# Optimization experiments

Measured on AMD Instinct MI355X. Metric: run time of the kernel, lower is better.

The kernel has to match this reference:

```python
import jax, jax.numpy as jnp
import numpy as np

B, C_IN, N = 8, 3, 4096
H = [64, 128, 256]      # local conv widths
G = [128, 64]           # global MLP widths
K = 16                  # kNN neighbors for edge_conv
EPS = 1e-5


def _ln(x, g, b):
    # LayerNorm(num_point): normalize over the last (point) axis per channel
    mu = jnp.mean(x, axis=-1, keepdims=True)
    var = jnp.mean((x - mu) ** 2, axis=-1, keepdims=True)
    return (x - mu) / jnp.sqrt(var + EPS) * g + b


def _conv_ln_relu(x, w, b, g, be):
    # 1x1 Conv1d == per-point matmul: [B,Cin,N] -> [B,Cout,N]
    x = jnp.einsum('oi,bin->bon', w, x) + b[None, :, None]
    return jax.nn.relu(_ln(x, g, be))


def _edge_conv(x):
    # DGCNN-style edge conv: kNN in feature space, max-aggregate neighbor feats
    f = jnp.swapaxes(x, 1, 2)                                  # [B,N,C]
    sq = jnp.sum(f * f, axis=-1)                               # [B,N]
    d = sq[:, :, None] + sq[:, None, :] - 2.0 * jnp.einsum('bnc,bmc->bnm', f, f)
    _, idx = jax.lax.top_k(-jax.lax.stop_gradient(d), K)       # [B,N,K]
    nbr = jax.vmap(lambda fb, ib: fb[ib])(f, idx)              # [B,N,K,C] gather
    return jnp.swapaxes(jnp.max(nbr, axis=2), 1, 2)            # [B,C,N]


def setup_inputs() -> dict:
    key = jax.random.key(0)
    ks = jax.random.split(key, 20)
    inp = {"point_cloud": jax.random.normal(ks[0], (B, C_IN, N), jnp.float32)}
    prev = C_IN
    for i, h in enumerate(H):
        inp[f"w{i}"] = jax.random.normal(ks[1 + 3 * i], (h, prev), jnp.float32) * (1.0 / np.sqrt(prev))
        inp[f"b{i}"] = jnp.zeros((h,), jnp.float32)
        inp[f"g{i}"] = jnp.ones((N,), jnp.float32)
        inp[f"be{i}"] = jnp.zeros((N,), jnp.float32)
        prev = h
    for i, h in enumerate(G + [1]):
        inp[f"gw{i}"] = jax.random.normal(ks[10 + i], (h, prev), jnp.float32) * (1.0 / np.sqrt(prev))
        inp[f"gb{i}"] = jnp.zeros((h,), jnp.float32)
        prev = h
    return inp


def reference(point_cloud, w0, b0, g0, be0, w1, b1, g1, be1, w2, b2, g2, be2,
              gw0, gb0, gw1, gb1, gw2, gb2):
    x = _conv_ln_relu(point_cloud, w0, b0, g0, be0)
    x = _conv_ln_relu(x, w1, b1, g1, be1)
    x = _conv_ln_relu(x, w2, b2, g2, be2)
    x = _edge_conv(x)                      # [B,256,N]
    pooled = jnp.mean(x, axis=2)           # mean over points (pnt_axis=2)
    h = jax.nn.relu(pooled @ gw0.T + gb0)
    h = jax.nn.relu(h @ gw1.T + gb1)
    return h @ gw2.T + gb2                 # [B,1] energy
```

## Files before the change

kernel.cpp:

```cpp
#include <hip/hip_runtime.h>
#include <stdint.h>

#define NPTS 4096
#define BATCH 8
#define KNN 16

typedef __attribute__((ext_vector_type(8))) short short8;
typedef __attribute__((ext_vector_type(4))) float f32x4;
typedef unsigned long long u64;

template<int CIN, int COTILE>
__global__ __launch_bounds__(256) void conv_kernel(
    const float* __restrict__ X, const float* __restrict__ W,
    const float* __restrict__ bias, float* __restrict__ Y, int cout) {
    int n = blockIdx.x * 256 + threadIdx.x;
    int co0 = blockIdx.y * COTILE;
    int b = blockIdx.z;
    const float* xb = X + (size_t)b * CIN * NPTS + n;
    float acc[COTILE];
#pragma unroll
    for (int j = 0; j < COTILE; ++j) acc[j] = bias[co0 + j];
    for (int ci = 0; ci < CIN; ++ci) {
        float xv = xb[(size_t)ci * NPTS];
#pragma unroll
        for (int j = 0; j < COTILE; ++j)
            acc[j] = fmaf(W[(co0 + j) * CIN + ci], xv, acc[j]);
    }
#pragma unroll
    for (int j = 0; j < COTILE; ++j)
        Y[((size_t)b * cout + co0 + j) * NPTS + n] = acc[j];
}

__global__ __launch_bounds__(256) void ln_relu_kernel(
    float* __restrict__ X, const float* __restrict__ g,
    const float* __restrict__ be, int C) {
    __shared__ float row_s[NPTS];
    __shared__ double sh[256], sh2[256];
    int c = blockIdx.x, b = blockIdx.y, t = threadIdx.x;
    float* row = X + ((size_t)b * C + c) * NPTS;
    double s = 0.0, s2 = 0.0;
    for (int i = t * 4; i < NPTS; i += 1024) {
        f32x4 v = *(const f32x4*)(row + i);
        *(f32x4*)(row_s + i) = v;
        s += (double)v.x + (double)v.y + (double)v.z + (double)v.w;
        s2 += (double)v.x * v.x + (double)v.y * v.y
            + (double)v.z * v.z + (double)v.w * v.w;
    }
    sh[t] = s; sh2[t] = s2;
    __syncthreads();
    for (int off = 128; off > 0; off >>= 1) {
        if (t < off) { sh[t] += sh[t + off]; sh2[t] += sh2[t + off]; }
        __syncthreads();
    }
    double mu = sh[0] / (double)NPTS;
    double var = sh2[0] / (double)NPTS - mu * mu;
    float rstd = (float)(1.0 / sqrt(var + 1e-5));
    float muf = (float)mu;
    for (int i = t * 4; i < NPTS; i += 1024) {
        f32x4 v = *(const f32x4*)(row_s + i);
        f32x4 gg = *(const f32x4*)(g + i);
        f32x4 bb = *(const f32x4*)(be + i);
        f32x4 o;
        o.x = fmaxf((v.x - muf) * rstd * gg.x + bb.x, 0.f);
        o.y = fmaxf((v.y - muf) * rstd * gg.y + bb.y, 0.f);
        o.z = fmaxf((v.z - muf) * rstd * gg.z + bb.z, 0.f);
        o.w = fmaxf((v.w - muf) * rstd * gg.w + bb.w, 0.f);
        *(f32x4*)(row + i) = o;
    }
}

#define ROW_E 72
#define ROW_B 144

__device__ inline unsigned short f2bf_rne(float x) {
    union { float f; unsigned u; } v; v.f = x;
    unsigned u = v.u;
    return (unsigned short)((u + 0x7FFFu + ((u >> 16) & 1u)) >> 16);
}

__global__ __launch_bounds__(256) void convert_kernel(
    const float* __restrict__ X2, unsigned short* __restrict__ Fc,
    float* __restrict__ SQ) {
    __shared__ float T[64][65];
    __shared__ float Q[64][4];
    int b = blockIdx.y;
    int n0 = blockIdx.x * 64;
    int t = threadIdx.x;
    int n_loc = t >> 2, cq = t & 3;
    float sacc = 0.f;
    for (int cc = 0; cc < 4; ++cc) {
        for (int r = 0; r < 16; ++r) {
            int cl = r * 4 + (t >> 6);
            T[cl][t & 63] = X2[((size_t)b * 256 + cc * 64 + cl) * NPTS + n0 + (t & 63)];
        }
        __syncthreads();
        size_t base = (((size_t)(b * 4 + cc) * NPTS) + n0 + n_loc) * ROW_E;
#pragma unroll
        for (int j = 0; j < 16; ++j) {
            int c = cq * 16 + j;
            float x = T[c][n_loc];
            sacc = fmaf(x, x, sacc);
            Fc[base + c] = f2bf_rne(x);
        }
        __syncthreads();
    }
    Q[n_loc][cq] = sacc;
    __syncthreads();
    if (t < 64)
        SQ[(size_t)b * NPTS + n0 + t] = Q[t][0] + Q[t][1] + Q[t][2] + Q[t][3];
}

#define A_BYTES (128 * ROW_B)
#define STAGE_BYTES (2 * A_BYTES)
#define SENT32 0xFFFFFFFFu

__device__ inline void async_cp16(const void* g, void* l) {
    __builtin_amdgcn_global_load_lds((const __attribute__((address_space(1))) void*)g,
                                     (__attribute__((address_space(3))) void*)l, 16, 0, 0);
}

__device__ inline unsigned flip_f(float d) {
    union { float f; unsigned u; } v; v.f = d;
    return v.u ^ (((unsigned)((int)v.u >> 31)) | 0x80000000u);
}
__device__ inline float unflip_f(unsigned y) {
    unsigned m = (~((unsigned)((int)y >> 31))) | 0x80000000u;
    union { unsigned u; float f; } v; v.u = y ^ m;
    return v.f;
}
__device__ inline float thr_of(unsigned p) {
    unsigned tb = p | 0xFFFu;
    if (tb >= 0xFF800000u) tb = 0xFF800000u;
    return unflip_f(tb);
}

__global__ __launch_bounds__(256) void knn_mfma_kernel(
    const unsigned short* __restrict__ Fc, const float* __restrict__ SQ,
    unsigned* __restrict__ DpA, unsigned* __restrict__ DpB) {
    __shared__ __align__(16) char smem[STAGE_BYTES];
    __shared__ float sq_ks[128];
    __shared__ float thrx[256];
    int b = blockIdx.x;
    int q0 = blockIdx.y * 128;
    int ks = blockIdx.z;
    int t = threadIdx.x;
    int lane = t & 63;
    int wv = t >> 6;
    int wq = wv & 1, wk = wv >> 1;
    int quad = lane >> 4;
    int l15 = lane & 15;
    const float* sqb = SQ + (size_t)b * NPTS;
    const char* FcB = (const char*)Fc + (size_t)b * 4 * NPTS * ROW_B;

    thrx[t] = __int_as_float(0x7F800000);

    unsigned lst[KNN];
#pragma unroll
    for (int j = 0; j < KNN; ++j) lst[j] = SENT32;
    float thr_part = __int_as_float(0x7F800000);

    int q = t & 127, sub = t >> 7;

    for (int kt = 0; kt < 8; ++kt) {
        int kbase = ks * 1024 + kt * 128;
        if (t < 128) sq_ks[t] = sqb[kbase + t];
        f32x4 acc[4][4];
#pragma unroll
        for (int i = 0; i < 4; ++i)
#pragma unroll
            for (int j = 0; j < 4; ++j) acc[i][j] = (f32x4){0.f, 0.f, 0.f, 0.f};

        for (int kc = 0; kc < 4; ++kc) {
            __syncthreads();
            const char* gA = FcB + ((size_t)kc * NPTS + q0) * ROW_B;
            const char* gB = FcB + ((size_t)kc * NPTS + kbase) * ROW_B;
#pragma unroll
            for (int i = 0; i < 9; ++i) {
                int chunk = (i * 4 + wv) * 1024;
                const char* g = (chunk < A_BYTES) ? (gA + chunk) : (gB + (chunk - A_BYTES));
                async_cp16(g + lane * 16, smem + chunk);
            }
            __syncthreads();
#pragma unroll
            for (int kss = 0; kss < 2; ++kss) {
                int coff = kss * 64 + quad * 16;
                short8 a[4], bf[4];
#pragma unroll
                for (int tq = 0; tq < 4; ++tq)
                    a[tq] = *(const short8*)(smem + (wq * 64 + tq * 16 + l15) * ROW_B + coff);
#pragma unroll
                for (int tk = 0; tk < 4; ++tk)
                    bf[tk] = *(const short8*)(smem + A_BYTES + (wk * 64 + tk * 16 + l15) * ROW_B + coff);
#pragma unroll
                for (int tq = 0; tq < 4; ++tq)
#pragma unroll
                    for (int tk = 0; tk < 4; ++tk)
                        acc[tq][tk] = __builtin_amdgcn_mfma_f32_16x16x32_bf16(
                            a[tq], bf[tk], acc[tq][tk], 0, 0, 0);
            }
        }

        float* Gd = (float*)smem;
        const float* gq = Gd + (size_t)q * 68 + sub * 32;
#pragma unroll 1
        for (int h = 0; h < 2; ++h) {
            __syncthreads();
            if (wk == h) {
#pragma unroll
                for (int tk = 0; tk < 4; ++tk) {
                    float sqk = sq_ks[h * 64 + tk * 16 + l15];
#pragma unroll
                    for (int tq = 0; tq < 4; ++tq) {
                        float* gp = Gd + (size_t)(wq * 64 + tq * 16 + quad * 4) * 68
                                  + tk * 16 + l15;
                        f32x4 g = acc[tq][tk];
                        gp[0]   = fmaf(-2.f, g.x, sqk);
                        gp[68]  = fmaf(-2.f, g.y, sqk);
                        gp[136] = fmaf(-2.f, g.z, sqk);
                        gp[204] = fmaf(-2.f, g.w, sqk);
                    }
                }
            }
            __syncthreads();
            if (h == 0) thr_part = thrx[t ^ 128];
            float thrf = fminf(thr_of(lst[KNN - 1]), thr_part);
            unsigned mask = 0;
#pragma unroll
            for (int i = 7; i >= 0; --i) {
                f32x4 v = *(const f32x4*)(gq + i * 4);
                mask = mask + mask + (unsigned)(v.w <= thrf);
                mask = mask + mask + (unsigned)(v.z <= thrf);
                mask = mask + mask + (unsigned)(v.y <= thrf);
                mask = mask + mask + (unsigned)(v.x <= thrf);
            }
            while (__any((int)(mask != 0u))) {
                if (mask) {
                    int j = __ffs(mask) - 1;
                    mask &= mask - 1u;
                    float d = gq[j];
                    unsigned pk = (flip_f(d) & 0xFFFFF000u)
                                | (unsigned)(kbase + h * 64 + sub * 32 + j);
                    if (pk < lst[KNN - 1]) {
                        lst[KNN - 1] = pk;
#pragma unroll
                        for (int s = KNN - 1; s > 0; --s) {
                            if (lst[s] < lst[s - 1]) {
                                unsigned tmp = lst[s]; lst[s] = lst[s - 1]; lst[s - 1] = tmp;
                            }
                        }
                    }
                }
            }
            if (h == 1) thrx[t] = thr_of(lst[KNN - 1]);
        }
    }

    __syncthreads();
    unsigned* mls = (unsigned*)smem;
#pragma unroll
    for (int j = 0; j < KNN; ++j) mls[t * 17 + j] = lst[j];
    __syncthreads();
    if (t < 128) {
        const unsigned* da = mls + t * 17;
        const unsigned* db = mls + (t + 128) * 17;
        unsigned* outp = ((ks < 2) ? DpA : DpB)
                       + ((size_t)((b * NPTS + q0 + t) * 2 + (ks & 1))) * KNN;
        int ia = 0, ib2 = 0;
        for (int k = 0; k < KNN; ++k) {
            bool ta = (ib2 >= KNN) || (ia < KNN && da[ia] < db[ib2]);
            outp[k] = ta ? da[ia++] : db[ib2++];
        }
    }
}

__global__ __launch_bounds__(256) void transpose_kernel(
    const float* __restrict__ X2, float* __restrict__ Xt) {
    __shared__ float T[64][65];
    int b = blockIdx.x;
    int n0 = blockIdx.y * 64;
    int t = threadIdx.x;
    int wave = t >> 6, lane = t & 63;
    for (int cc = 0; cc < 4; ++cc) {
        for (int r = 0; r < 16; ++r) {
            int cl = r * 4 + (t >> 6);
            T[cl][t & 63] = X2[((size_t)b * 256 + cc * 64 + cl) * NPTS + n0 + (t & 63)];
        }
        __syncthreads();
#pragma unroll
        for (int r = 0; r < 16; ++r) {
            int n_l = wave * 16 + r;
            Xt[((size_t)b * NPTS + n0 + n_l) * 256 + cc * 64 + lane] = T[lane][n_l];
        }
        __syncthreads();
    }
}

__global__ __launch_bounds__(256) void gather_pool_kernel(
    const float* __restrict__ Xt, const unsigned* __restrict__ DpA,
    const unsigned* __restrict__ DpB, float* __restrict__ Pp) {
    __shared__ int idxs[16][KNN];
    int b = blockIdx.x, blk = blockIdx.y;
    int t = threadIdx.x;
    if (t < 16) {
        int qg = b * NPTS + blk * 16 + t;
        const unsigned* L0 = DpA + (size_t)qg * 2 * KNN;
        const unsigned* L1 = L0 + KNN;
        const unsigned* L2 = DpB + (size_t)qg * 2 * KNN;
        const unsigned* L3 = L2 + KNN;
        int p0 = 0, p1 = 0, p2 = 0, p3 = 0;
#pragma unroll 1
        for (int k = 0; k < KNN; ++k) {
            unsigned v0 = (p0 < KNN) ? L0[p0] : SENT32;
            unsigned v1 = (p1 < KNN) ? L1[p1] : SENT32;
            unsigned v2 = (p2 < KNN) ? L2[p2] : SENT32;
            unsigned v3 = (p3 < KNN) ? L3[p3] : SENT32;
            unsigned best = v0; int bl = 0;
            if (v1 < best) { best = v1; bl = 1; }
            if (v2 < best) { best = v2; bl = 2; }
            if (v3 < best) { best = v3; bl = 3; }
            idxs[t][k] = (int)(best & 0xFFFu);
            if (bl == 0) ++p0; else if (bl == 1) ++p1; else if (bl == 2) ++p2; else ++p3;
        }
    }
    __syncthreads();
    int wv = t >> 6, lane = t & 63;
    const float* xb = Xt + (size_t)b * NPTS * 256;
    f32x4 sum = (f32x4){0.f, 0.f, 0.f, 0.f};
#pragma unroll 1
    for (int i = 0; i < 4; ++i) {
        const int* idp = idxs[wv * 4 + i];
        f32x4 m = *(const f32x4*)(xb + (size_t)idp[0] * 256 + lane * 4);
#pragma unroll
        for (int k = 1; k < KNN; ++k) {
            f32x4 v = *(const f32x4*)(xb + (size_t)idp[k] * 256 + lane * 4);
            m.x = fmaxf(m.x, v.x); m.y = fmaxf(m.y, v.y);
            m.z = fmaxf(m.z, v.z); m.w = fmaxf(m.w, v.w);
        }
        sum.x += m.x; sum.y += m.y; sum.z += m.z; sum.w += m.w;
    }
    __shared__ float S[4][256];
    *(f32x4*)&S[wv][lane * 4] = sum;
    __syncthreads();
    Pp[((size_t)b * 256 + blk) * 256 + t] = S[0][t] + S[1][t] + S[2][t] + S[3][t];
}

__global__ __launch_bounds__(256) void pool_mlp_kernel(
    const float* __restrict__ Pp,
    const float* __restrict__ gw0, const float* __restrict__ gb0,
    const float* __restrict__ gw1, const float* __restrict__ gb1,
    const float* __restrict__ gw2, const float* __restrict__ gb2,
    float* __restrict__ out) {
    __shared__ float P[256];
    __shared__ float h1[128];
    __shared__ float h2[64];
    int b = blockIdx.x, t = threadIdx.x;
    double s = 0.0;
#pragma unroll 4
    for (int j = 0; j < 256; ++j) s += (double)Pp[((size_t)b * 256 + j) * 256 + t];
    P[t] = (float)(s / (double)NPTS);
    __syncthreads();
    if (t < 128) {
        const float* w = gw0 + t * 256;
        double acc = 0.0;
        for (int c = 0; c < 256; ++c) acc += (double)P[c] * (double)w[c];
        float v = gb0[t] + (float)acc;
        h1[t] = v > 0.f ? v : 0.f;
    }
    __syncthreads();
    if (t < 64) {
        const float* w = gw1 + t * 128;
        double acc = 0.0;
        for (int c = 0; c < 128; ++c) acc += (double)h1[c] * (double)w[c];
        float v = gb1[t] + (float)acc;
        h2[t] = v > 0.f ? v : 0.f;
    }
    __syncthreads();
    if (t == 0) {
        double acc = 0.0;
        for (int c = 0; c < 64; ++c) acc += (double)h2[c] * (double)gw2[c];
        out[b] = gb2[0] + (float)acc;
    }
}

extern "C" void kernel_launch(void* const* d_in, const int* in_sizes, int n_in,
                              void* d_out, int out_size, void* d_ws, size_t ws_size,
                              hipStream_t stream) {
    const float* pc  = (const float*)d_in[0];
    const float* w0  = (const float*)d_in[1];
    const float* b0  = (const float*)d_in[2];
    const float* g0  = (const float*)d_in[3];
    const float* be0 = (const float*)d_in[4];
    const float* w1  = (const float*)d_in[5];
    const float* b1  = (const float*)d_in[6];
    const float* g1  = (const float*)d_in[7];
    const float* be1 = (const float*)d_in[8];
    const float* w2  = (const float*)d_in[9];
    const float* b2  = (const float*)d_in[10];
    const float* g2  = (const float*)d_in[11];
    const float* be2 = (const float*)d_in[12];
    const float* gw0 = (const float*)d_in[13];
    const float* gb0 = (const float*)d_in[14];
    const float* gw1 = (const float*)d_in[15];
    const float* gb1 = (const float*)d_in[16];
    const float* gw2 = (const float*)d_in[17];
    const float* gb2 = (const float*)d_in[18];
    float* out = (float*)d_out;

    float* ws = (float*)d_ws;
    float* X0 = ws;
    float* X2 = X0 + 2097152;
    float* R  = X2 + 8388608;
    float* X1 = R;
    unsigned short* Fc = (unsigned short*)R;
    float* Xt = R;
    unsigned* DpA = (unsigned*)X0;
    unsigned* DpB = (unsigned*)(R + 9437184);
    float* SQ = R + 11534336;
    float* P  = SQ + 32768;
    float* Pp = P + 2048;

    conv_kernel<3, 16><<<dim3(NPTS / 256, 64 / 16, BATCH), 256, 0, stream>>>(pc, w0, b0, X0, 64);
    ln_relu_kernel<<<dim3(64, BATCH), 256, 0, stream>>>(X0, g0, be0, 64);
    conv_kernel<64, 32><<<dim3(NPTS / 256, 128 / 32, BATCH), 256, 0, stream>>>(X0, w1, b1, X1, 128);
    ln_relu_kernel<<<dim3(128, BATCH), 256, 0, stream>>>(X1, g1, be1, 128);
    conv_kernel<128, 64><<<dim3(NPTS / 256, 256 / 64, BATCH), 256, 0, stream>>>(X1, w2, b2, X2, 256);
    ln_relu_kernel<<<dim3(256, BATCH), 256, 0, stream>>>(X2, g2, be2, 256);

    convert_kernel<<<dim3(NPTS / 64, BATCH), 256, 0, stream>>>(X2, Fc, SQ);
    knn_mfma_kernel<<<dim3(BATCH, 32, 4), 256, 0, stream>>>(Fc, SQ, DpA, DpB);
    transpose_kernel<<<dim3(BATCH, NPTS / 64), 256, 0, stream>>>(X2, Xt);
    gather_pool_kernel<<<dim3(BATCH, 256), 256, 0, stream>>>(Xt, DpA, DpB, Pp);
    pool_mlp_kernel<<<dim3(BATCH), 256, 0, stream>>>(Pp, gw0, gb0, gw1, gb1, gw2, gb2, out);
}
```

Baseline: 543.3 us.

## Fuse 1x1 conv with LayerNorm+ReLU, keeping channel rows in shared memory

Replaces the separate conv and LN/ReLU kernels with one kernel per layer. Each block computes G full output rows (all 4096 points) for one batch into LDS, then normalizes each row and writes the final activation. This removes the intermediate global write and reread of pre-norm activations and cuts the launches from six to three. In exchange the grid is much smaller (256 to 512 blocks), each block uses G*16KB of LDS, which limits occupancy, and the input rows are reread once per channel group.

Result: faster. 502.6 us (-7.5%).

```diff
diff --git a/kernel.cpp b/kernel.cpp
--- a/kernel.cpp
+++ b/kernel.cpp
@@ -9,63 +9,77 @@
 typedef __attribute__((ext_vector_type(4))) float f32x4;
 typedef unsigned long long u64;
 
-template<int CIN, int COTILE>
-__global__ __launch_bounds__(256) void conv_kernel(
+template<int CIN, int G>
+__global__ __launch_bounds__(256) void conv_ln_kernel(
     const float* __restrict__ X, const float* __restrict__ W,
-    const float* __restrict__ bias, float* __restrict__ Y, int cout) {
-    int n = blockIdx.x * 256 + threadIdx.x;
-    int co0 = blockIdx.y * COTILE;
-    int b = blockIdx.z;
-    const float* xb = X + (size_t)b * CIN * NPTS + n;
-    float acc[COTILE];
-#pragma unroll
-    for (int j = 0; j < COTILE; ++j) acc[j] = bias[co0 + j];
-    for (int ci = 0; ci < CIN; ++ci) {
-        float xv = xb[(size_t)ci * NPTS];
-#pragma unroll
-        for (int j = 0; j < COTILE; ++j)
-            acc[j] = fmaf(W[(co0 + j) * CIN + ci], xv, acc[j]);
-    }
-#pragma unroll
-    for (int j = 0; j < COTILE; ++j)
-        Y[((size_t)b * cout + co0 + j) * NPTS + n] = acc[j];
-}
-
-__global__ __launch_bounds__(256) void ln_relu_kernel(
-    float* __restrict__ X, const float* __restrict__ g,
-    const float* __restrict__ be, int C) {
-    __shared__ float row_s[NPTS];
+    const float* __restrict__ bias, const float* __restrict__ g,
+    const float* __restrict__ be, float* __restrict__ Y, int cout) {
+    __shared__ float rows[G * NPTS];
     __shared__ double sh[256], sh2[256];
-    int c = blockIdx.x, b = blockIdx.y, t = threadIdx.x;
-    float* row = X + ((size_t)b * C + c) * NPTS;
-    double s = 0.0, s2 = 0.0;
-    for (int i = t * 4; i < NPTS; i += 1024) {
-        f32x4 v = *(const f32x4*)(row + i);
-        *(f32x4*)(row_s + i) = v;
-        s += (double)v.x + (double)v.y + (double)v.z + (double)v.w;
-        s2 += (double)v.x * v.x + (double)v.y * v.y
-            + (double)v.z * v.z + (double)v.w * v.w;
-    }
-    sh[t] = s; sh2[t] = s2;
-    __syncthreads();
-    for (int off = 128; off > 0; off >>= 1) {
-        if (t < off) { sh[t] += sh[t + off]; sh2[t] += sh2[t + off]; }
-        __syncthreads();
-    }
-    double mu = sh[0] / (double)NPTS;
-    double var = sh2[0] / (double)NPTS - mu * mu;
-    float rstd = (float)(1.0 / sqrt(var + 1e-5));
-    float muf = (float)mu;
-    for (int i = t * 4; i < NPTS; i += 1024) {
-        f32x4 v = *(const f32x4*)(row_s + i);
-        f32x4 gg = *(const f32x4*)(g + i);
-        f32x4 bb = *(const f32x4*)(be + i);
-        f32x4 o;
-        o.x = fmaxf((v.x - muf) * rstd * gg.x + bb.x, 0.f);
-        o.y = fmaxf((v.y - muf) * rstd * gg.y + bb.y, 0.f);
-        o.z = fmaxf((v.z - muf) * rstd * gg.z + bb.z, 0.f);
-        o.w = fmaxf((v.w - muf) * rstd * gg.w + bb.w, 0.f);
-        *(f32x4*)(row + i) = o;
+    int b = blockIdx.x;
+    int co0 = blockIdx.y * G;
+    int t = threadIdx.x;
+    const float* xb = X + (size_t)b * CIN * NPTS;
+
+#pragma unroll 1
+    for (int chunk = 0; chunk < 4; ++chunk) {
+        int n = chunk * 1024 + t * 4;
+        f32x4 acc[G];
+#pragma unroll
+        for (int j = 0; j < G; ++j) {
+            float bj = bias[co0 + j];
+            acc[j] = (f32x4){bj, bj, bj, bj};
+        }
+        for (int ci = 0; ci < CIN; ++ci) {
+            f32x4 xv = *(const f32x4*)(xb + (size_t)ci * NPTS + n);
+#pragma unroll
+            for (int j = 0; j < G; ++j) {
+                float w = W[(co0 + j) * CIN + ci];
+                acc[j].x = fmaf(w, xv.x, acc[j].x);
+                acc[j].y = fmaf(w, xv.y, acc[j].y);
+                acc[j].z = fmaf(w, xv.z, acc[j].z);
+                acc[j].w = fmaf(w, xv.w, acc[j].w);
+            }
+        }
+#pragma unroll
+        for (int j = 0; j < G; ++j)
+            *(f32x4*)(rows + j * NPTS + n) = acc[j];
+    }
+    __syncthreads();
+
+#pragma unroll 1
+    for (int j = 0; j < G; ++j) {
+        float* row = rows + j * NPTS;
+        double s = 0.0, s2 = 0.0;
+        for (int i = t * 4; i < NPTS; i += 1024) {
+            f32x4 v = *(const f32x4*)(row + i);
+            s += (double)v.x + (double)v.y + (double)v.z + (double)v.w;
+            s2 += (double)v.x * v.x + (double)v.y * v.y
+                + (double)v.z * v.z + (double)v.w * v.w;
+        }
+        sh[t] = s; sh2[t] = s2;
+        __syncthreads();
+        for (int off = 128; off > 0; off >>= 1) {
+            if (t < off) { sh[t] += sh[t + off]; sh2[t] += sh2[t + off]; }
+            __syncthreads();
+        }
+        double mu = sh[0] / (double)NPTS;
+        double var = sh2[0] / (double)NPTS - mu * mu;
+        float rstd = (float)(1.0 / sqrt(var + 1e-5));
+        float muf = (float)mu;
+        float* yrow = Y + ((size_t)b * cout + co0 + j) * NPTS;
+        for (int i = t * 4; i < NPTS; i += 1024) {
+            f32x4 v = *(const f32x4*)(row + i);
+            f32x4 gg = *(const f32x4*)(g + i);
+            f32x4 bb = *(const f32x4*)(be + i);
+            f32x4 o;
+            o.x = fmaxf((v.x - muf) * rstd * gg.x + bb.x, 0.f);
+            o.y = fmaxf((v.y - muf) * rstd * gg.y + bb.y, 0.f);
+            o.z = fmaxf((v.z - muf) * rstd * gg.z + bb.z, 0.f);
+            o.w = fmaxf((v.w - muf) * rstd * gg.w + bb.w, 0.f);
+            *(f32x4*)(yrow + i) = o;
+        }
+        __syncthreads();
     }
 }
 
@@ -419,12 +433,12 @@
     float* P  = SQ + 32768;
     float* Pp = P + 2048;
 
-    conv_kernel<3, 16><<<dim3(NPTS / 256, 64 / 16, BATCH), 256, 0, stream>>>(pc, w0, b0, X0, 64);
-    ln_relu_kernel<<<dim3(64, BATCH), 256, 0, stream>>>(X0, g0, be0, 64);
-    conv_kernel<64, 32><<<dim3(NPTS / 256, 128 / 32, BATCH), 256, 0, stream>>>(X0, w1, b1, X1, 128);
-    ln_relu_kernel<<<dim3(128, BATCH), 256, 0, stream>>>(X1, g1, be1, 128);
-    conv_kernel<128, 64><<<dim3(NPTS / 256, 256 / 64, BATCH), 256, 0, stream>>>(X1, w2, b2, X2, 256);
-    ln_relu_kernel<<<dim3(256, BATCH), 256, 0, stream>>>(X2, g2, be2, 256);
+    conv_ln_kernel<3, 2><<<dim3(BATCH, 64 / 2), 256, 0, stream>>>(
+        pc, w0, b0, g0, be0, X0, 64);
+    conv_ln_kernel<64, 4><<<dim3(BATCH, 128 / 4), 256, 0, stream>>>(
+        X0, w1, b1, g1, be1, X1, 128);
+    conv_ln_kernel<128, 4><<<dim3(BATCH, 256 / 4), 256, 0, stream>>>(
+        X1, w2, b2, g2, be2, X2, 256);
 
     convert_kernel<<<dim3(NPTS / 64, BATCH), 256, 0, stream>>>(X2, Fc, SQ);
     knn_mfma_kernel<<<dim3(BATCH, 32, 4), 256, 0, stream>>>(Fc, SQ, DpA, DpB);
```
